# Kernel optimization log

Hardware: AMD Instinct MI355X
Metric: run time of the kernel (lower is better)

Reference implementation:

```python
import jax, jax.numpy as jnp
import numpy as np

N = 20000       # nodes
E = 160000      # edges (avg degree 8)
NFEAT = 512
NHID = 512
NCLASS = 64
NLAYERS = 4


def setup_inputs() -> dict:
    key = jax.random.key(0)
    ks = jax.random.split(key, 9)
    s = 0.05
    x = jax.random.normal(ks[0], (N, NFEAT), dtype=jnp.float32)
    edge_index = jax.random.randint(ks[1], (2, E), 0, N, dtype=jnp.int64)
    W_enc = jax.random.normal(ks[2], (NFEAT, NHID), dtype=jnp.float32) * s
    b_enc = jnp.zeros((NHID,), dtype=jnp.float32)
    W_convs = jax.random.normal(ks[3], (NLAYERS, NHID, NHID), dtype=jnp.float32) * s
    b_convs = jnp.zeros((NLAYERS, NHID), dtype=jnp.float32)
    W_dec = jax.random.normal(ks[4], (NHID, NCLASS), dtype=jnp.float32) * s
    b_dec = jnp.zeros((NCLASS,), dtype=jnp.float32)
    return {"x": x, "edge_index": edge_index, "W_enc": W_enc, "b_enc": b_enc,
            "W_convs": W_convs, "b_convs": b_convs, "W_dec": W_dec, "b_dec": b_dec}


def reference(x, edge_index, W_enc, b_enc, W_convs, b_convs, W_dec, b_dec):
    n = x.shape[0]
    loops = jnp.arange(n, dtype=edge_index.dtype)
    # GCNConv adds self-loops, then sym-normalizes: D^-1/2 (A+I) D^-1/2
    src = jnp.concatenate([edge_index[0], loops])  # [E+N]
    dst = jnp.concatenate([edge_index[1], loops])  # [E+N]
    deg = jax.ops.segment_sum(jnp.ones_like(dst, dtype=x.dtype), dst, num_segments=N)
    dinv = jnp.where(deg > 0, jax.lax.rsqrt(deg), jnp.zeros_like(deg))
    norm = (dinv[src] * dinv[dst])[:, None]  # [E+N, 1]

    # encoder: relu(Linear)
    h = jax.nn.relu(x @ W_enc + b_enc)

    def gcn_step(h, wb):
        W, b = wb
        hW = h @ W                                   # [N, H]
        msg = hW[src] * norm                         # gather + scale
        agg = jax.ops.segment_sum(msg, dst, num_segments=N)  # scatter-add
        return jax.nn.relu(agg + b), None            # bias after aggregation (PyG)

    h, _ = jax.lax.scan(gcn_step, h, (W_convs, b_convs))

    # decoder (dropout p=0 in eval -> identity)
    return h @ W_dec + b_dec
```

## Files before the change

### kernel.cpp

```cpp
#include <hip/hip_runtime.h>

#define N_NODES 20000
#define E_EDGES 160000
#define NFEAT   512
#define NHID    512
#define NCLASS  64
#define NLAYERS 4

#define SCAN_CHUNK 1024
#define NBLK ((N_NODES + SCAN_CHUNK - 1) / SCAN_CHUNK)
#define CNT_BLOCKS ((E_EDGES + 255) / 256)

using bf16x8 = __attribute__((ext_vector_type(8))) short;
using f32x4  = __attribute__((ext_vector_type(4))) float;
using u16x8  = __attribute__((ext_vector_type(8))) unsigned short;

__device__ __forceinline__ unsigned short f2bf(float f) {
    union { float f; unsigned int u; } v; v.f = f;
    unsigned int u = v.u + 0x7FFFu + ((v.u >> 16) & 1u);
    return (unsigned short)(u >> 16);
}
__device__ __forceinline__ float bf2f(unsigned short h) {
    union { unsigned int u; float f; } v; v.u = ((unsigned int)h) << 16;
    return v.f;
}
__device__ __forceinline__ void gl2lds16(const void* gptr, void* lptr) {
    __builtin_amdgcn_global_load_lds(
        (const __attribute__((address_space(1))) unsigned int*)gptr,
        (__attribute__((address_space(3))) unsigned int*)lptr,
        16, 0, 0);
}

__global__ __launch_bounds__(256) void prep_all(const int* __restrict__ dst,
                                                int* __restrict__ counts,
                                                int* __restrict__ bsums,
                                                const float* __restrict__ W_enc,
                                                const float* __restrict__ W_convs,
                                                const float* __restrict__ W_dec,
                                                unsigned short* __restrict__ WencT,
                                                unsigned short* __restrict__ WcvT,
                                                unsigned short* __restrict__ WdecT) {
    __shared__ int bins[NBLK];
    __shared__ float tile[32][33];
    const int b = blockIdx.x, t = threadIdx.x;

    if (b < CNT_BLOCKS) {
        if (t < NBLK) bins[t] = 0;
        __syncthreads();
        const int e = b * 256 + t;
        if (e < E_EDGES) {
            const int d = dst[e];
            atomicAdd(&counts[d], 1);
            atomicAdd(&bins[d >> 10], 1);
        }
        __syncthreads();
        if (t < NBLK && bins[t]) atomicAdd(&bsums[t], bins[t]);
        return;
    }

    const int bid = b - CNT_BLOCKS;
    const int id  = bid >> 8;
    const int rem = bid & 255;
    const int n0  = (rem & 15) * 32;
    const int k0  = (rem >> 4) * 32;
    const float* W; unsigned short* WT; int N;
    const int K = 512;
    if (id == 0)            { W = W_enc; WT = WencT; N = NHID; }
    else if (id <= NLAYERS) { W = W_convs + (size_t)(id - 1) * NHID * NHID;
                              WT = WcvT  + (size_t)(id - 1) * NHID * NHID; N = NHID; }
    else                    { W = W_dec; WT = WdecT; N = NCLASS; }
    if (n0 >= N) return;
    const int tx = t & 31, ty = t >> 5;
#pragma unroll
    for (int i = 0; i < 32; i += 8)
        tile[ty + i][tx] = W[(size_t)(k0 + ty + i) * N + n0 + tx];
    __syncthreads();
#pragma unroll
    for (int i = 0; i < 32; i += 8)
        WT[(size_t)(n0 + ty + i) * K + k0 + tx] = f2bf(tile[tx][ty + i]);
}

__global__ __launch_bounds__(64) void scan_bsums(const int* __restrict__ bsums,
                                                 int* __restrict__ boffs) {
    const int t = threadIdx.x;
    const int orig = (t < NBLK) ? bsums[t] : 0;
    int v = orig;
    for (int off = 1; off < 64; off <<= 1) {
        int u = __shfl_up(v, off, 64);
        if (t >= off) v += u;
    }
    if (t < NBLK) boffs[t] = v - orig;
}

__global__ __launch_bounds__(256) void write_rowptr(const int* __restrict__ counts,
                                                    const int* __restrict__ boffs,
                                                    int* __restrict__ row_ptr,
                                                    int* __restrict__ cursor,
                                                    float* __restrict__ dinv) {
    __shared__ int part[256];
    const int b = blockIdx.x, t = threadIdx.x;
    const int base = b * SCAN_CHUNK + t * 4;
    int c[4], s = 0;
    for (int i = 0; i < 4; ++i) {
        int idx = base + i;
        c[i] = (idx < N_NODES) ? counts[idx] : 0;
        s += c[i];
    }
    part[t] = s;
    __syncthreads();
    for (int off = 1; off < 256; off <<= 1) {
        int v = (t >= off) ? part[t - off] : 0;
        __syncthreads();
        part[t] += v;
        __syncthreads();
    }
    int run = boffs[b] + ((t == 0) ? 0 : part[t - 1]);
    for (int i = 0; i < 4; ++i) {
        int idx = base + i;
        if (idx < N_NODES) {
            row_ptr[idx] = run;
            cursor[idx]  = run;
            dinv[idx]    = rsqrtf((float)c[i] + 1.0f);
            run += c[i];
        }
    }
    if (b == 0 && t == 0) row_ptr[N_NODES] = E_EDGES;
}

__global__ __launch_bounds__(256) void csr_fill(const int* __restrict__ src,
                                                const int* __restrict__ dst,
                                                const float* __restrict__ dinv,
                                                int* __restrict__ cursor,
                                                int2* __restrict__ ew) {
    int e = blockIdx.x * 256 + threadIdx.x;
    if (e < E_EDGES) {
        int s = src[e], d = dst[e];
        int pos = atomicAdd(&cursor[d], 1);
        ew[pos] = make_int2(s, __float_as_int(dinv[s] * dinv[d]));
    }
    if (e < 8) ew[E_EDGES + e] = make_int2(0, 0);
}

template <int BM, int BN, int WR, int WC, bool RELU, bool HASBIAS, bool OUTBF16, bool A32>
__global__ __launch_bounds__(256) void gemm_mfma(const void* __restrict__ Aptr,
                                                 const unsigned short* __restrict__ BT,
                                                 const float* __restrict__ bias,
                                                 void* __restrict__ Cout,
                                                 int M, int N, int K) {
    constexpr int BK = 32;
    constexpr int R  = BM / (16 * WR);
    constexpr int C  = BN / (16 * WC);
    constexpr int RA = (BM * BK) / (256 * 8);
    constexpr int RB = (BN * BK) / (256 * 8);
    __shared__ unsigned short lA[BM * BK];
    __shared__ unsigned short lB[BN * BK];

    const int t    = threadIdx.x;
    const int lane = t & 63;
    const int wv   = t >> 6;
    const int wr   = wv / WC;
    const int wc   = wv % WC;
    const int lm   = lane & 15;
    const int quad = lane >> 4;

    const int MBLK = (M + BM - 1) / BM;
    const int NBN  = N / BN;
    int mblk, nblk;
    {
        const int i    = blockIdx.x;
        const int full = (MBLK / 8) * 8 * NBN;
        if (i < full) {
            const int g = i / (8 * NBN);
            const int l = i % (8 * NBN);
            mblk = g * 8 + (l & 7);
            nblk = l >> 3;
        } else {
            const int t2  = i - full;
            const int rem = MBLK - (MBLK / 8) * 8;
            mblk = (MBLK / 8) * 8 + t2 % rem;
            nblk = t2 / rem;
        }
    }
    const int m0 = mblk * BM;
    const int n0 = nblk * BN;

    f32x4 acc[R][C] = {};

    for (int kt = 0; kt < K; kt += BK) {
#pragma unroll
        for (int i = 0; i < RA; ++i) {
            int idx = i * 256 + t;
            int row = idx >> 2;
            int kof = (idx & 3) << 3;
            int gr = m0 + row; if (gr >= M) gr = M - 1;
            if constexpr (!A32) {
                gl2lds16((const unsigned short*)Aptr + (size_t)gr * K + kt + kof,
                         &lA[idx * 8]);
            } else {
                const float* p = (const float*)Aptr + (size_t)gr * K + kt + kof;
                float4 f0 = *(const float4*)p;
                float4 f1 = *(const float4*)(p + 4);
                u16x8 pk;
                pk[0] = f2bf(f0.x); pk[1] = f2bf(f0.y);
                pk[2] = f2bf(f0.z); pk[3] = f2bf(f0.w);
                pk[4] = f2bf(f1.x); pk[5] = f2bf(f1.y);
                pk[6] = f2bf(f1.z); pk[7] = f2bf(f1.w);
                *(u16x8*)&lA[idx * 8] = pk;
            }
        }
#pragma unroll
        for (int i = 0; i < RB; ++i) {
            int idx = i * 256 + t;
            int row = idx >> 2;
            int kof = (idx & 3) << 3;
            gl2lds16(BT + (size_t)(n0 + row) * K + kt + kof, &lB[idx * 8]);
        }
        __syncthreads();

        bf16x8 af[R], bfr[C];
#pragma unroll
        for (int r = 0; r < R; ++r)
            af[r] = *(const bf16x8*)&lA[(wr * R * 16 + r * 16 + lm) * BK + quad * 8];
#pragma unroll
        for (int c = 0; c < C; ++c)
            bfr[c] = *(const bf16x8*)&lB[(wc * C * 16 + c * 16 + lm) * BK + quad * 8];
#pragma unroll
        for (int r = 0; r < R; ++r)
#pragma unroll
            for (int c = 0; c < C; ++c)
                acc[r][c] = __builtin_amdgcn_mfma_f32_16x16x32_bf16(af[r], bfr[c],
                                                                    acc[r][c], 0, 0, 0);
        __syncthreads();
    }

#pragma unroll
    for (int r = 0; r < R; ++r) {
#pragma unroll
        for (int c = 0; c < C; ++c) {
            const int colg = n0 + wc * C * 16 + c * 16 + lm;
            const float bb = HASBIAS ? bias[colg] : 0.0f;
            const int rowb = m0 + wr * R * 16 + r * 16 + quad * 4;
#pragma unroll
            for (int i = 0; i < 4; ++i) {
                const int rr = rowb + i;
                if (rr < M) {
                    float v = acc[r][c][i] + bb;
                    if (RELU) v = fmaxf(v, 0.0f);
                    if (OUTBF16)
                        ((unsigned short*)Cout)[(size_t)rr * N + colg] = f2bf(v);
                    else
                        ((float*)Cout)[(size_t)rr * N + colg] = v;
                }
            }
        }
    }
}

__global__ __launch_bounds__(256) void gcn_aggregate(const unsigned short* __restrict__ hW,
                                                     const int* __restrict__ row_ptr,
                                                     const int2* __restrict__ ew,
                                                     const float* __restrict__ dinv,
                                                     const float* __restrict__ bias,
                                                     unsigned short* __restrict__ out) {
    const int wv   = threadIdx.x >> 6;
    const int lane = threadIdx.x & 63;
    int d = blockIdx.x * 4 + wv;
    d = __builtin_amdgcn_readfirstlane(d);
    if (d >= N_NODES) return;
    const int beg = __builtin_amdgcn_readfirstlane(row_ptr[d]);
    const int end = __builtin_amdgcn_readfirstlane(row_ptr[d + 1]);
    const size_t foff = (size_t)lane * 8;

    const float di = dinv[d];
    const float sl = di * di;
    u16x8 sv = *(const u16x8*)(hW + (size_t)d * NHID + foff);
    float acc[8];
#pragma unroll
    for (int i = 0; i < 8; ++i) acc[i] = bf2f(sv[i]) * sl;

    for (int j = beg; j < end; j += 8) {
        int   sK[8];
        float wK[8];
        u16x8 v[8];
#pragma unroll
        for (int k = 0; k < 8; ++k) {
            const int jj = j + k;
            const int2 e = ew[jj];
            const bool valid = jj < end;
            sK[k] = valid ? e.x : 0;
            wK[k] = valid ? __int_as_float(e.y) : 0.0f;
        }
#pragma unroll
        for (int k = 0; k < 8; ++k)
            v[k] = *(const u16x8*)(hW + (size_t)sK[k] * NHID + foff);
#pragma unroll
        for (int k = 0; k < 8; ++k)
#pragma unroll
            for (int i = 0; i < 8; ++i)
                acc[i] += bf2f(v[k][i]) * wK[k];
    }

    const float4 b0v = *(const float4*)(bias + foff);
    const float4 b1v = *(const float4*)(bias + foff + 4);
    u16x8 r;
    r[0] = f2bf(fmaxf(acc[0] + b0v.x, 0.0f));
    r[1] = f2bf(fmaxf(acc[1] + b0v.y, 0.0f));
    r[2] = f2bf(fmaxf(acc[2] + b0v.z, 0.0f));
    r[3] = f2bf(fmaxf(acc[3] + b0v.w, 0.0f));
    r[4] = f2bf(fmaxf(acc[4] + b1v.x, 0.0f));
    r[5] = f2bf(fmaxf(acc[5] + b1v.y, 0.0f));
    r[6] = f2bf(fmaxf(acc[6] + b1v.z, 0.0f));
    r[7] = f2bf(fmaxf(acc[7] + b1v.w, 0.0f));
    *(u16x8*)(out + (size_t)d * NHID + foff) = r;
}

extern "C" void kernel_launch(void* const* d_in, const int* in_sizes, int n_in,
                              void* d_out, int out_size, void* d_ws, size_t ws_size,
                              hipStream_t stream) {
    const float* x       = (const float*)d_in[0];
    const int*   ei      = (const int*)d_in[1];
    const float* W_enc   = (const float*)d_in[2];
    const float* b_enc   = (const float*)d_in[3];
    const float* W_convs = (const float*)d_in[4];
    const float* b_convs = (const float*)d_in[5];
    const float* W_dec   = (const float*)d_in[6];
    const float* b_dec   = (const float*)d_in[7];
    float* out = (float*)d_out;

    const int* src = ei;
    const int* dst = ei + E_EDGES;

    char* ws = (char*)d_ws;
    auto alloc = [&](size_t bytes) {
        char* p = ws;
        ws += (bytes + 255) / 256 * 256;
        return p;
    };
    float* dinv     = (float*)alloc(N_NODES * 4);
    int*   counts   = (int*)  alloc((N_NODES + NBLK) * 4);
    int*   bsums    = counts + N_NODES;
    int*   row_ptr  = (int*)  alloc((N_NODES + 1) * 4);
    int*   cursor   = (int*)  alloc(N_NODES * 4);
    int*   boffs    = (int*)  alloc(NBLK * 4);
    int2*  ew       = (int2*) alloc((E_EDGES + 8) * 8);
    unsigned short* WencT = (unsigned short*)alloc((size_t)NFEAT * NHID * 2);
    unsigned short* WcvT  = (unsigned short*)alloc((size_t)NLAYERS * NHID * NHID * 2);
    unsigned short* WdecT = (unsigned short*)alloc((size_t)NHID * NCLASS * 2);
    unsigned short* B1    = (unsigned short*)alloc((size_t)N_NODES * NHID * 2);
    unsigned short* B2    = (unsigned short*)alloc((size_t)N_NODES * NHID * 2);

    hipMemsetAsync(counts, 0, (N_NODES + NBLK) * sizeof(int), stream);
    prep_all<<<CNT_BLOCKS + 6 * 256, 256, 0, stream>>>(
        dst, counts, bsums, W_enc, W_convs, W_dec, WencT, WcvT, WdecT);
    scan_bsums<<<1, 64, 0, stream>>>(bsums, boffs);
    write_rowptr<<<NBLK, 256, 0, stream>>>(counts, boffs, row_ptr, cursor, dinv);
    csr_fill<<<(E_EDGES + 255) / 256, 256, 0, stream>>>(src, dst, dinv, cursor, ew);

    const int MBLK64 = (N_NODES + 63) / 64;

    gemm_mfma<64, 128, 2, 2, true, true, true, true>
        <<<MBLK64 * (NHID / 128), 256, 0, stream>>>(
        x, WencT, b_enc, B1, N_NODES, NHID, NFEAT);

    for (int L = 0; L < NLAYERS; ++L) {
        gemm_mfma<64, 128, 2, 2, false, false, true, false>
            <<<MBLK64 * (NHID / 128), 256, 0, stream>>>(
            B1, WcvT + (size_t)L * NHID * NHID, nullptr, B2, N_NODES, NHID, NHID);
        gcn_aggregate<<<(N_NODES + 3) / 4, 256, 0, stream>>>(
            B2, row_ptr, ew, dinv, b_convs + (size_t)L * NHID, B1);
    }

    gemm_mfma<64, 64, 2, 2, false, true, false, false>
        <<<MBLK64 * (NCLASS / 64), 256, 0, stream>>>(
        B1, WdecT, b_dec, out, N_NODES, NCLASS, NHID);
}
```

Measured before the change: 337.5 us.

## Double-buffer GEMM LDS tiles with register prefetch and padded row stride

Replaces the direct global-to-LDS loads in the MFMA GEMM with register-staged loads of the next K tile, issued before the current tile's MFMAs and written to a second LDS buffer afterwards. This overlaps global memory latency with compute and drops one barrier per iteration. It also pads the LDS row stride to BK+8 to reduce bank conflicts on fragment reads. In exchange it doubles LDS use, adds VGPR pressure for the staging registers, and adds extra ds_write instructions.

```diff
diff --git a/kernel.cpp b/kernel.cpp
--- a/kernel.cpp
+++ b/kernel.cpp
@@ -23,12 +23,6 @@
 __device__ __forceinline__ float bf2f(unsigned short h) {
     union { unsigned int u; float f; } v; v.u = ((unsigned int)h) << 16;
     return v.f;
-}
-__device__ __forceinline__ void gl2lds16(const void* gptr, void* lptr) {
-    __builtin_amdgcn_global_load_lds(
-        (const __attribute__((address_space(1))) unsigned int*)gptr,
-        (__attribute__((address_space(3))) unsigned int*)lptr,
-        16, 0, 0);
 }
 
 __global__ __launch_bounds__(256) void prep_all(const int* __restrict__ dst,
@@ -147,13 +141,14 @@
                                                  const float* __restrict__ bias,
                                                  void* __restrict__ Cout,
                                                  int M, int N, int K) {
-    constexpr int BK = 32;
-    constexpr int R  = BM / (16 * WR);
-    constexpr int C  = BN / (16 * WC);
-    constexpr int RA = (BM * BK) / (256 * 8);
-    constexpr int RB = (BN * BK) / (256 * 8);
-    __shared__ unsigned short lA[BM * BK];
-    __shared__ unsigned short lB[BN * BK];
+    constexpr int BK  = 32;
+    constexpr int LDK = BK + 8;
+    constexpr int R   = BM / (16 * WR);
+    constexpr int C   = BN / (16 * WC);
+    constexpr int RA  = (BM * BK) / (256 * 8);
+    constexpr int RB  = (BN * BK) / (256 * 8);
+    __shared__ unsigned short lA[2][BM * LDK];
+    __shared__ unsigned short lB[2][BN * LDK];
 
     const int t    = threadIdx.x;
     const int lane = t & 63;
@@ -184,18 +179,17 @@
     const int m0 = mblk * BM;
     const int n0 = nblk * BN;
 
-    f32x4 acc[R][C] = {};
-
-    for (int kt = 0; kt < K; kt += BK) {
+    u16x8 aR[RA], bR[RB];
+
+    auto gload = [&](int kt) {
 #pragma unroll
         for (int i = 0; i < RA; ++i) {
-            int idx = i * 256 + t;
-            int row = idx >> 2;
-            int kof = (idx & 3) << 3;
+            const int idx = i * 256 + t;
+            const int row = idx >> 2, kof = (idx & 3) << 3;
             int gr = m0 + row; if (gr >= M) gr = M - 1;
             if constexpr (!A32) {
-                gl2lds16((const unsigned short*)Aptr + (size_t)gr * K + kt + kof,
-                         &lA[idx * 8]);
+                aR[i] = *(const u16x8*)((const unsigned short*)Aptr +
+                                        (size_t)gr * K + kt + kof);
             } else {
                 const float* p = (const float*)Aptr + (size_t)gr * K + kt + kof;
                 float4 f0 = *(const float4*)p;
@@ -205,31 +199,56 @@
                 pk[2] = f2bf(f0.z); pk[3] = f2bf(f0.w);
                 pk[4] = f2bf(f1.x); pk[5] = f2bf(f1.y);
                 pk[6] = f2bf(f1.z); pk[7] = f2bf(f1.w);
-                *(u16x8*)&lA[idx * 8] = pk;
+                aR[i] = pk;
             }
         }
 #pragma unroll
         for (int i = 0; i < RB; ++i) {
-            int idx = i * 256 + t;
-            int row = idx >> 2;
-            int kof = (idx & 3) << 3;
-            gl2lds16(BT + (size_t)(n0 + row) * K + kt + kof, &lB[idx * 8]);
-        }
-        __syncthreads();
+            const int idx = i * 256 + t;
+            const int row = idx >> 2, kof = (idx & 3) << 3;
+            bR[i] = *(const u16x8*)(BT + (size_t)(n0 + row) * K + kt + kof);
+        }
+    };
+    auto dswrite = [&](int buf) {
+#pragma unroll
+        for (int i = 0; i < RA; ++i) {
+            const int idx = i * 256 + t;
+            const int row = idx >> 2, kof = (idx & 3) << 3;
+            *(u16x8*)&lA[buf][row * LDK + kof] = aR[i];
+        }
+#pragma unroll
+        for (int i = 0; i < RB; ++i) {
+            const int idx = i * 256 + t;
+            const int row = idx >> 2, kof = (idx & 3) << 3;
+            *(u16x8*)&lB[buf][row * LDK + kof] = bR[i];
+        }
+    };
+
+    f32x4 acc[R][C] = {};
+
+    gload(0);
+    dswrite(0);
+    __syncthreads();
+
+    const int NIT = K / BK;
+    for (int it = 0; it < NIT; ++it) {
+        const int cur = it & 1;
+        if (it + 1 < NIT) gload((it + 1) * BK);
 
         bf16x8 af[R], bfr[C];
 #pragma unroll
         for (int r = 0; r < R; ++r)
-            af[r] = *(const bf16x8*)&lA[(wr * R * 16 + r * 16 + lm) * BK + quad * 8];
+            af[r] = *(const bf16x8*)&lA[cur][(wr * R * 16 + r * 16 + lm) * LDK + quad * 8];
 #pragma unroll
         for (int c = 0; c < C; ++c)
-            bfr[c] = *(const bf16x8*)&lB[(wc * C * 16 + c * 16 + lm) * BK + quad * 8];
+            bfr[c] = *(const bf16x8*)&lB[cur][(wc * C * 16 + c * 16 + lm) * LDK + quad * 8];
 #pragma unroll
         for (int r = 0; r < R; ++r)
 #pragma unroll
             for (int c = 0; c < C; ++c)
                 acc[r][c] = __builtin_amdgcn_mfma_f32_16x16x32_bf16(af[r], bfr[c],
                                                                     acc[r][c], 0, 0, 0);
+        if (it + 1 < NIT) dswrite(cur ^ 1);
         __syncthreads();
     }
 
```

Measured after the change: 345.1 us. 2.3% more time.

## Load GEMM fragments directly from global into registers with double buffering

Applied to the files above, without the earlier changes.

The MFMA GEMM no longer stages A and B tiles through LDS. Each lane loads its bf16x8 fragments straight from global memory into registers, and a two-stage register double buffer prefetches the next K step while the current one computes. K is now a compile-time template parameter, so the K loop fully unrolls. This removes the LDS traffic and the block-wide barriers. In exchange, each wave re-reads A and B rows that other waves also read, which relies on L1/L2 for reuse and raises global load traffic and register pressure.

```diff
diff --git a/kernel.cpp b/kernel.cpp
--- a/kernel.cpp
+++ b/kernel.cpp
@@ -23,12 +23,6 @@
 __device__ __forceinline__ float bf2f(unsigned short h) {
     union { unsigned int u; float f; } v; v.u = ((unsigned int)h) << 16;
     return v.f;
-}
-__device__ __forceinline__ void gl2lds16(const void* gptr, void* lptr) {
-    __builtin_amdgcn_global_load_lds(
-        (const __attribute__((address_space(1))) unsigned int*)gptr,
-        (__attribute__((address_space(3))) unsigned int*)lptr,
-        16, 0, 0);
 }
 
 __global__ __launch_bounds__(256) void prep_all(const int* __restrict__ dst,
@@ -141,19 +135,17 @@
     if (e < 8) ew[E_EDGES + e] = make_int2(0, 0);
 }
 
-template <int BM, int BN, int WR, int WC, bool RELU, bool HASBIAS, bool OUTBF16, bool A32>
+template <int KT, int BM, int BN, int WR, int WC,
+          bool RELU, bool HASBIAS, bool OUTBF16, bool A32>
 __global__ __launch_bounds__(256) void gemm_mfma(const void* __restrict__ Aptr,
                                                  const unsigned short* __restrict__ BT,
                                                  const float* __restrict__ bias,
                                                  void* __restrict__ Cout,
-                                                 int M, int N, int K) {
-    constexpr int BK = 32;
-    constexpr int R  = BM / (16 * WR);
-    constexpr int C  = BN / (16 * WC);
-    constexpr int RA = (BM * BK) / (256 * 8);
-    constexpr int RB = (BN * BK) / (256 * 8);
-    __shared__ unsigned short lA[BM * BK];
-    __shared__ unsigned short lB[BN * BK];
+                                                 int M, int N) {
+    constexpr int BK  = 32;
+    constexpr int NIT = KT / BK;
+    constexpr int R   = BM / (16 * WR);
+    constexpr int C   = BN / (16 * WC);
 
     const int t    = threadIdx.x;
     const int lane = t & 63;
@@ -184,20 +176,28 @@
     const int m0 = mblk * BM;
     const int n0 = nblk * BN;
 
-    f32x4 acc[R][C] = {};
-
-    for (int kt = 0; kt < K; kt += BK) {
-#pragma unroll
-        for (int i = 0; i < RA; ++i) {
-            int idx = i * 256 + t;
-            int row = idx >> 2;
-            int kof = (idx & 3) << 3;
-            int gr = m0 + row; if (gr >= M) gr = M - 1;
+    int arow[R];
+#pragma unroll
+    for (int r = 0; r < R; ++r) {
+        int rr = m0 + wr * R * 16 + r * 16 + lm;
+        arow[r] = (rr < M) ? rr : (M - 1);
+    }
+    int brow[C];
+#pragma unroll
+    for (int c = 0; c < C; ++c)
+        brow[c] = n0 + wc * C * 16 + c * 16 + lm;
+
+    const int q8 = quad * 8;
+
+    bf16x8 Af[2][R], Bf[2][C];
+    auto loadstep = [&](int s, int kt) {
+#pragma unroll
+        for (int r = 0; r < R; ++r) {
             if constexpr (!A32) {
-                gl2lds16((const unsigned short*)Aptr + (size_t)gr * K + kt + kof,
-                         &lA[idx * 8]);
+                Af[s][r] = *(const bf16x8*)((const unsigned short*)Aptr +
+                                            (size_t)arow[r] * KT + kt + q8);
             } else {
-                const float* p = (const float*)Aptr + (size_t)gr * K + kt + kof;
+                const float* p = (const float*)Aptr + (size_t)arow[r] * KT + kt + q8;
                 float4 f0 = *(const float4*)p;
                 float4 f1 = *(const float4*)(p + 4);
                 u16x8 pk;
@@ -205,32 +205,26 @@
                 pk[2] = f2bf(f0.z); pk[3] = f2bf(f0.w);
                 pk[4] = f2bf(f1.x); pk[5] = f2bf(f1.y);
                 pk[6] = f2bf(f1.z); pk[7] = f2bf(f1.w);
-                *(u16x8*)&lA[idx * 8] = pk;
+                Af[s][r] = (bf16x8)pk;
             }
         }
 #pragma unroll
-        for (int i = 0; i < RB; ++i) {
-            int idx = i * 256 + t;
-            int row = idx >> 2;
-            int kof = (idx & 3) << 3;
-            gl2lds16(BT + (size_t)(n0 + row) * K + kt + kof, &lB[idx * 8]);
-        }
-        __syncthreads();
-
-        bf16x8 af[R], bfr[C];
+        for (int c = 0; c < C; ++c)
+            Bf[s][c] = *(const bf16x8*)(BT + (size_t)brow[c] * KT + kt + q8);
+    };
+
+    f32x4 acc[R][C] = {};
+    loadstep(0, 0);
+#pragma unroll
+    for (int it = 0; it < NIT; ++it) {
+        if (it + 1 < NIT) loadstep((it + 1) & 1, (it + 1) * BK);
+        const int s = it & 1;
 #pragma unroll
         for (int r = 0; r < R; ++r)
-            af[r] = *(const bf16x8*)&lA[(wr * R * 16 + r * 16 + lm) * BK + quad * 8];
-#pragma unroll
-        for (int c = 0; c < C; ++c)
-            bfr[c] = *(const bf16x8*)&lB[(wc * C * 16 + c * 16 + lm) * BK + quad * 8];
-#pragma unroll
-        for (int r = 0; r < R; ++r)
 #pragma unroll
             for (int c = 0; c < C; ++c)
-                acc[r][c] = __builtin_amdgcn_mfma_f32_16x16x32_bf16(af[r], bfr[c],
+                acc[r][c] = __builtin_amdgcn_mfma_f32_16x16x32_bf16(Af[s][r], Bf[s][c],
                                                                     acc[r][c], 0, 0, 0);
-        __syncthreads();
     }
 
 #pragma unroll
@@ -358,19 +352,19 @@
 
     const int MBLK64 = (N_NODES + 63) / 64;
 
-    gemm_mfma<64, 128, 2, 2, true, true, true, true>
+    gemm_mfma<512, 64, 128, 2, 2, true, true, true, true>
         <<<MBLK64 * (NHID / 128), 256, 0, stream>>>(
-        x, WencT, b_enc, B1, N_NODES, NHID, NFEAT);
+        x, WencT, b_enc, B1, N_NODES, NHID);
 
     for (int L = 0; L < NLAYERS; ++L) {
-        gemm_mfma<64, 128, 2, 2, false, false, true, false>
+        gemm_mfma<512, 64, 128, 2, 2, false, false, true, false>
             <<<MBLK64 * (NHID / 128), 256, 0, stream>>>(
-            B1, WcvT + (size_t)L * NHID * NHID, nullptr, B2, N_NODES, NHID, NHID);
+            B1, WcvT + (size_t)L * NHID * NHID, nullptr, B2, N_NODES, NHID);
         gcn_aggregate<<<(N_NODES + 3) / 4, 256, 0, stream>>>(
             B2, row_ptr, ew, dinv, b_convs + (size_t)L * NHID, B1);
     }
 
-    gemm_mfma<64, 64, 2, 2, false, true, false, false>
+    gemm_mfma<512, 64, 64, 2, 2, false, true, false, false>
         <<<MBLK64 * (NCLASS / 64), 256, 0, stream>>>(
-        B1, WdecT, b_dec, out, N_NODES, NCLASS, NHID);
-}
+        B1, WdecT, b_dec, out, N_NODES, NCLASS);
+}
```

Measured after the change: 542.3 us. 1.61x slower.

## Double-buffer GEMM LDS tiles and widen K-tile to 64

Applied to the files above, without the earlier changes.

The MFMA GEMM now uses two LDS buffers per operand, and the K tile grows from 32 to 64. The next tile is loaded into the spare buffer while MFMAs run on the current one, so only one barrier is needed per iteration. This aims to hide global-to-LDS latency and halve the number of barriers. In exchange, LDS use per block is four times larger, which may reduce occupancy. The wider rows also keep the same non-swizzled layout, so LDS bank conflicts may change.

```diff
diff --git a/kernel.cpp b/kernel.cpp
--- a/kernel.cpp
+++ b/kernel.cpp
@@ -147,13 +147,14 @@
                                                  const float* __restrict__ bias,
                                                  void* __restrict__ Cout,
                                                  int M, int N, int K) {
-    constexpr int BK = 32;
+    constexpr int BK = 64;
     constexpr int R  = BM / (16 * WR);
     constexpr int C  = BN / (16 * WC);
     constexpr int RA = (BM * BK) / (256 * 8);
     constexpr int RB = (BN * BK) / (256 * 8);
-    __shared__ unsigned short lA[BM * BK];
-    __shared__ unsigned short lB[BN * BK];
+    constexpr int CH = BK / 8;
+    __shared__ unsigned short lA[2][BM * BK];
+    __shared__ unsigned short lB[2][BN * BK];
 
     const int t    = threadIdx.x;
     const int lane = t & 63;
@@ -184,18 +185,16 @@
     const int m0 = mblk * BM;
     const int n0 = nblk * BN;
 
-    f32x4 acc[R][C] = {};
-
-    for (int kt = 0; kt < K; kt += BK) {
+    auto stage = [&](int kt, int buf) {
 #pragma unroll
         for (int i = 0; i < RA; ++i) {
-            int idx = i * 256 + t;
-            int row = idx >> 2;
-            int kof = (idx & 3) << 3;
+            const int idx = i * 256 + t;
+            const int row = idx / CH;
+            const int kof = (idx % CH) << 3;
             int gr = m0 + row; if (gr >= M) gr = M - 1;
             if constexpr (!A32) {
                 gl2lds16((const unsigned short*)Aptr + (size_t)gr * K + kt + kof,
-                         &lA[idx * 8]);
+                         &lA[buf][idx * 8]);
             } else {
                 const float* p = (const float*)Aptr + (size_t)gr * K + kt + kof;
                 float4 f0 = *(const float4*)p;
@@ -205,31 +204,44 @@
                 pk[2] = f2bf(f0.z); pk[3] = f2bf(f0.w);
                 pk[4] = f2bf(f1.x); pk[5] = f2bf(f1.y);
                 pk[6] = f2bf(f1.z); pk[7] = f2bf(f1.w);
-                *(u16x8*)&lA[idx * 8] = pk;
+                *(u16x8*)&lA[buf][idx * 8] = pk;
             }
         }
 #pragma unroll
         for (int i = 0; i < RB; ++i) {
-            int idx = i * 256 + t;
-            int row = idx >> 2;
-            int kof = (idx & 3) << 3;
-            gl2lds16(BT + (size_t)(n0 + row) * K + kt + kof, &lB[idx * 8]);
-        }
-        __syncthreads();
-
-        bf16x8 af[R], bfr[C];
-#pragma unroll
-        for (int r = 0; r < R; ++r)
-            af[r] = *(const bf16x8*)&lA[(wr * R * 16 + r * 16 + lm) * BK + quad * 8];
-#pragma unroll
-        for (int c = 0; c < C; ++c)
-            bfr[c] = *(const bf16x8*)&lB[(wc * C * 16 + c * 16 + lm) * BK + quad * 8];
-#pragma unroll
-        for (int r = 0; r < R; ++r)
+            const int idx = i * 256 + t;
+            const int row = idx / CH;
+            const int kof = (idx % CH) << 3;
+            gl2lds16(BT + (size_t)(n0 + row) * K + kt + kof, &lB[buf][idx * 8]);
+        }
+    };
+
+    f32x4 acc[R][C] = {};
+
+    stage(0, 0);
+    __syncthreads();
+
+    const int NIT = K / BK;
+    for (int it = 0; it < NIT; ++it) {
+        const int cur = it & 1;
+        if (it + 1 < NIT) stage((it + 1) * BK, cur ^ 1);
+
+#pragma unroll
+        for (int kk = 0; kk < BK; kk += 32) {
+            bf16x8 af[R], bfr[C];
+#pragma unroll
+            for (int r = 0; r < R; ++r)
+                af[r] = *(const bf16x8*)&lA[cur][(wr * R * 16 + r * 16 + lm) * BK + kk + quad * 8];
 #pragma unroll
             for (int c = 0; c < C; ++c)
-                acc[r][c] = __builtin_amdgcn_mfma_f32_16x16x32_bf16(af[r], bfr[c],
-                                                                    acc[r][c], 0, 0, 0);
+                bfr[c] = *(const bf16x8*)&lB[cur][(wc * C * 16 + c * 16 + lm) * BK + kk + quad * 8];
+#pragma unroll
+            for (int r = 0; r < R; ++r)
+#pragma unroll
+                for (int c = 0; c < C; ++c)
+                    acc[r][c] = __builtin_amdgcn_mfma_f32_16x16x32_bf16(af[r], bfr[c],
+                                                                        acc[r][c], 0, 0, 0);
+        }
         __syncthreads();
     }
 
```

After: 364.6 us. +8.0%, slower.
